# Kernel tuning notes

Measured on AMD Instinct MI355X. Metric: run time of the kernel, lower is better.

The kernel has to match this reference:

```python
import jax, jax.numpy as jnp
import numpy as np

B, S, D, H = 2, 4096, 128, 128
EPS = 1e-6
NEG_INF = -1e30


def _complex_linear(xr, xi, Wr, Wi, br, bi):
    # x: (B,S,D); W: (H,D); complex linear (Wr + i Wi)(xr + i xi) + (br + i bi) per layer math:
    # real_out = (xr Wr + br) - (xi Wi + bi); imag_out = (xi Wr + br) + (xr Wi + bi)
    out_r = xr @ Wr.T + br - (xi @ Wi.T + bi)
    out_i = xi @ Wr.T + br + (xr @ Wi.T + bi)
    return out_r, out_i


def setup_inputs() -> dict:
    key = jax.random.key(0)
    ks = jax.random.split(key, 24)
    scale = 1.0 / np.sqrt(D)
    def W(k):
        return jax.random.normal(k, (H, D), jnp.float32) * scale
    def b(k):
        return jax.random.normal(k, (H,), jnp.float32) * 0.01
    inp = {
        "Z_q": jax.random.normal(ks[0], (B, 2, S, D, 1), jnp.float32),
        "Z_k": jax.random.normal(ks[1], (B, 2, S, D, 1), jnp.float32),
        "Z_v": jax.random.normal(ks[2], (B, 2, S, D, 1), jnp.float32),
        "Wq_r": W(ks[3]), "Wq_i": W(ks[4]), "bq_r": b(ks[5]), "bq_i": b(ks[6]),
        "Wk_r": W(ks[7]), "Wk_i": W(ks[8]), "bk_r": b(ks[9]), "bk_i": b(ks[10]),
        "Wv_r": W(ks[11]), "Wv_i": W(ks[12]), "bv_r": b(ks[13]), "bv_i": b(ks[14]),
        "Wp_r": W(ks[15]), "Wp_i": W(ks[16]), "bp_r": b(ks[17]), "bp_i": b(ks[18]),
        "noise_floor": jnp.asarray(1.0, jnp.float32),
        "tau": jnp.asarray(0.0, jnp.float32),
    }
    return inp


def reference(Z_q, Z_k, Z_v,
              Wq_r, Wq_i, bq_r, bq_i,
              Wk_r, Wk_i, bk_r, bk_i,
              Wv_r, Wv_i, bv_r, bv_i,
              Wp_r, Wp_i, bp_r, bp_i,
              noise_floor, tau):
    # squeeze trailing singleton; split real/imag -> (B,S,D)
    zqr, zqi = Z_q[:, 0, :, :, 0], Z_q[:, 1, :, :, 0]
    zkr, zki = Z_k[:, 0, :, :, 0], Z_k[:, 1, :, :, 0]
    zvr, zvi = Z_v[:, 0, :, :, 0], Z_v[:, 1, :, :, 0]

    Qr, Qi = _complex_linear(zqr, zqi, Wq_r, Wq_i, bq_r, bq_i)
    Kr, Ki = _complex_linear(zkr, zki, Wk_r, Wk_i, bk_r, bk_i)
    Vr, Vi = _complex_linear(zvr, zvi, Wv_r, Wv_i, bv_r, bv_i)

    # InverseMahalanobis: R2[b,i,j] = sum_h |Q[b,i]-K[b,j]|^2
    q2 = jnp.sum(Qr * Qr + Qi * Qi, axis=-1)          # (B,S)
    k2 = jnp.sum(Kr * Kr + Ki * Ki, axis=-1)          # (B,S)
    re_qk = (jnp.einsum('bsh,bth->bst', Qr, Kr)
             + jnp.einsum('bsh,bth->bst', Qi, Ki))    # (B,S,S)
    R2 = q2[:, :, None] + k2[:, None, :] - 2.0 * re_qk

    attn_scores = -jax.nn.softplus(tau) * jnp.log(noise_floor ** 2 + R2 + EPS)
    mask = jnp.tril(jnp.ones((S, S), dtype=bool))[None]
    attn_scores = jnp.where(mask, attn_scores, NEG_INF)
    attn_weights = jax.nn.softmax(attn_scores / jnp.sqrt(jnp.float32(H)), axis=-1)

    # attn (real) times complex V
    est_r = jnp.einsum('bst,bth->bsh', attn_weights, Vr)
    est_i = jnp.einsum('bst,bth->bsh', attn_weights, Vi)

    out_r, out_i = _complex_linear(est_r, est_i, Wp_r, Wp_i, bp_r, bp_i)
    out = jnp.stack((out_r, out_i), axis=1)[..., None]  # (B,2,S,H,1)
    return out, attn_weights
```

## Files before the change

kernel.cpp:

```cpp
#include <hip/hip_runtime.h>

#define S_LEN 4096
#define NBATCH 2
#define ROWS (NBATCH*S_LEN)
#define OUT_ELEMS 2097152

typedef _Float16 f16;
typedef _Float16 f16x8 __attribute__((ext_vector_type(8)));
typedef _Float16 f16x4 __attribute__((ext_vector_type(4)));
typedef float f32x4 __attribute__((ext_vector_type(4)));

#define MT_OFF    0x000000
#define BIAS_OFF  0x080000
#define SC_OFF    0x081000
#define QH_OFF    0x100000
#define KH_OFF    0x500000
#define VT_OFF    0x900000
#define Q2_OFF    0xD00000
#define K2_OFF    0xD10000
#define L_OFF     0xD20000
#define EST_OFF   0xE00000
#define PW_OFF    0x1600000
#define WS_NEED   0x5600000

#define MFMA16(A,B,C) __builtin_amdgcn_mfma_f32_16x16x32_f16(A,B,C,0,0,0)

__device__ __forceinline__ void async_cp16(f16* lds, const f16* g) {
  __builtin_amdgcn_global_load_lds(
      (const __attribute__((address_space(1))) void*)g,
      (__attribute__((address_space(3))) void*)lds, 16, 0, 0);
}


template<int TR>
__device__ __forceinline__ void stage16(f16* lds, const f16* g, int stride, int tid) {
#pragma unroll
  for (int i = 0; i < TR/64; ++i) {
    int idx = i*256 + tid;
    int row = idx >> 2;
    int c = (idx & 3) ^ ((row >> 1) & 3);
    async_cp16(lds + idx*8, g + (size_t)row*stride + c*8);
  }
}

template<int TR>
__device__ __forceinline__ void stage32(f16* lds, const float* g, int stride, int tid,
                                        const float* rowscale) {
#pragma unroll
  for (int i = 0; i < TR/32; ++i) {
    int idx = i*256 + tid;
    int row = idx >> 3, c = idx & 7;
    const float4* gp = (const float4*)(g + (size_t)row*stride + c*4);
    float4 v = *gp;
    float sc = rowscale ? rowscale[row] : 1.0f;
    f16x4 h; h[0]=(f16)(v.x*sc); h[1]=(f16)(v.y*sc); h[2]=(f16)(v.z*sc); h[3]=(f16)(v.w*sc);
    int slot = (((c >> 1) ^ ((row >> 1) & 3)) << 3) + (c & 1)*4;
    *(f16x4*)(lds + row*32 + slot) = h;
  }
}

template<int MI, int NJ>
__device__ __forceinline__ void mfma_step(const f16* Asm, const f16* Bsm, int lane,
                                          int wm, int wn, f32x4 (&acc)[MI][NJ]) {
  f16x8 a[MI], b[NJ];
  int rr = lane & 15, kc = lane >> 4;
#pragma unroll
  for (int i=0;i<MI;i++) {
    int m = wm + i*16 + rr;
    a[i] = *(const f16x8*)(Asm + m*32 + ((kc ^ ((m>>1)&3)) << 3));
  }
#pragma unroll
  for (int j=0;j<NJ;j++) {
    int n = wn + j*16 + rr;
    b[j] = *(const f16x8*)(Bsm + n*32 + ((kc ^ ((n>>1)&3)) << 3));
  }
#pragma unroll
  for (int i=0;i<MI;i++)
#pragma unroll
    for (int j=0;j<NJ;j++) acc[i][j] = MFMA16(a[i], b[j], acc[i][j]);
}

__global__ __launch_bounds__(256)
void k_build(const float* Wqr, const float* Wqi, const float* bqr, const float* bqi,
             const float* Wkr, const float* Wki, const float* bkr, const float* bki,
             const float* Wvr, const float* Wvi, const float* bvr, const float* bvi,
             const float* Wpr, const float* Wpi, const float* bpr, const float* bpi,
             f16* Mt, float* bias) {
  int mat = blockIdx.x;
  const float *Wr, *Wi, *br, *bi;
  if (mat == 0)      { Wr=Wqr; Wi=Wqi; br=bqr; bi=bqi; }
  else if (mat == 1) { Wr=Wkr; Wi=Wki; br=bkr; bi=bki; }
  else if (mat == 2) { Wr=Wvr; Wi=Wvi; br=bvr; bi=bvi; }
  else               { Wr=Wpr; Wi=Wpi; br=bpr; bi=bpi; }
  int idx = blockIdx.y*256 + threadIdx.x;
  int n = idx >> 8, k = idx & 255;
  int d = k & 127, h = n & 127;
  float w = (k < 128) ? ((n < 128) ? Wr[h*128+d] : Wi[h*128+d])
                      : ((n < 128) ? -Wi[h*128+d] : Wr[h*128+d]);
  Mt[mat*65536 + n*256 + k] = (f16)w;
  if (k == 0)
    bias[mat*256 + n] = (n < 128) ? (br[n] - bi[n]) : (br[n-128] + bi[n-128]);
}

__global__ __launch_bounds__(256)
void k_init(float* est, float* zreg, float* sc, const float* nf, const float* tau) {
  int idx = blockIdx.x*256 + threadIdx.x;
  if (idx < 524288) ((float4*)est)[idx] = make_float4(0.f,0.f,0.f,0.f);
  else { int j = idx - 524288; if (j < 12288) ((float4*)zreg)[j] = make_float4(0.f,0.f,0.f,0.f); }
  if (idx == 0) {
    float t = tau[0];
    float c = __builtin_log2f(1.0f + __builtin_exp2f(t * 1.4426950408889634f))
              * 0.6931471805599453f;
    sc[0] = -c * 0.08838834764831845f;
    sc[1] = nf[0]*nf[0] + 1e-6f;
  }
}

__global__ __launch_bounds__(256)
void k_proj(const float* Zq, const float* Zk, const float* Zv,
            const f16* Mt, const float* bias,
            f16* Qh, f16* Kh, f16* Vt, float* q2, float* k2) {
  __shared__ f16 Asm[64*32];
  __shared__ f16 Bsm[128*32];
  __shared__ float bias_s[128];
  int tid = threadIdx.x;
  int mode = blockIdx.z;
  int m0 = blockIdx.x * 64, n0 = blockIdx.y * 128;
  const float* Z = (mode==0) ? Zq : (mode==1 ? Zk : Zv);
  const f16* Bt = Mt + mode*65536;
  if (tid < 128) bias_s[tid] = bias[mode*256 + n0 + tid];
  int b = m0 >> 12, s0 = m0 & 4095;
  int lane = tid & 63, w = tid >> 6;
  int wm = (w >> 1)*32, wn = (w & 1)*64;
  f32x4 acc[2][4] = {};
  for (int kb = 0; kb < 8; ++kb) {
    int k0 = kb*32;
    int part = k0 >> 7, d0 = k0 & 127;
    const float* Ag = Z + (((size_t)(b*2 + part))*S_LEN + s0)*128 + d0;
    stage32<64>(Asm, Ag, 128, tid, nullptr);
    stage16<128>(Bsm, Bt + n0*256 + k0, 256, tid);
    __syncthreads();
    mfma_step<2,4>(Asm, Bsm, lane, wm, wn, acc);
    __syncthreads();
  }
  int rr = (lane>>4)*4, cc = lane & 15;
  if (mode < 2) {
    f16* O = (mode==0) ? Qh : Kh;
    float rs[2][4];
#pragma unroll
    for (int i=0;i<2;i++)
#pragma unroll
      for (int r=0;r<4;r++) rs[i][r]=0.f;
#pragma unroll
    for (int i=0;i<2;i++)
#pragma unroll
      for (int j=0;j<4;j++) {
        int cl = wn + j*16 + cc;
        int cg = n0 + cl;
        float bv = bias_s[cl];
#pragma unroll
        for (int r=0;r<4;r++) {
          int rg = m0 + wm + i*16 + rr + r;
          f16 hv = (f16)(acc[i][j][r] + bv);
          O[(size_t)rg*256 + cg] = hv;
          float fv = (float)hv;
          rs[i][r] += fv*fv;
        }
      }
#pragma unroll
    for (int m=8;m>=1;m>>=1)
#pragma unroll
      for (int i=0;i<2;i++)
#pragma unroll
        for (int r=0;r<4;r++) rs[i][r] += __shfl_xor(rs[i][r], m, 64);
    if (cc == 0) {
      float* T = (mode==0) ? q2 : k2;
#pragma unroll
      for (int i=0;i<2;i++)
#pragma unroll
        for (int r=0;r<4;r++) {
          int rg = m0 + wm + i*16 + rr + r;
          atomicAdd(&T[rg], rs[i][r]);
        }
    }
  } else {
#pragma unroll
    for (int i=0;i<2;i++) {
      int t0 = s0 + wm + i*16 + rr;
#pragma unroll
      for (int j=0;j<4;j++) {
        int cl = wn + j*16 + cc;
        int cg = n0 + cl;
        float bv = bias_s[cl];
        f16x4 h4;
#pragma unroll
        for (int r=0;r<4;r++) h4[r] = (f16)(acc[i][j][r] + bv);
        *(f16x4*)(Vt + (size_t)b*1048576 + (size_t)cg*4096 + t0) = h4;
      }
    }
  }
}

__global__ __launch_bounds__(256)
void k_attn(const f16* Qh, const f16* Kh, const float* q2, const float* k2,
            const float* sc, float* lsum, f16* Pws) {
  __shared__ f16 Asm[128*32];
  __shared__ f16 Bsm[128*32];
  __shared__ float q2s[128], k2s[128];
  int x = blockIdx.x;
  int b = x / 528, r = x % 528;
  int sb = (int)((__builtin_sqrtf(8.f*(float)r + 1.f) - 1.f)*0.5f);
  while ((sb+1)*(sb+2)/2 <= r) sb++;
  while (sb*(sb+1)/2 > r) sb--;
  int tb = r - sb*(sb+1)/2;
  int s0 = sb*128, t0 = tb*128;
  int tid = threadIdx.x;
  if (tid < 128) {
    q2s[tid] = q2[b*S_LEN + s0 + tid];
    k2s[tid] = k2[b*S_LEN + t0 + tid];
  }
  float kc = sc[0], nf2 = sc[1];
  int lane = tid & 63, w = tid >> 6;
  int wm = (w >> 1)*64, wn = (w & 1)*64;
  const f16* Ag = Qh + ((size_t)(b*S_LEN) + s0)*256;
  const f16* Bg = Kh + ((size_t)(b*S_LEN) + t0)*256;
  f32x4 acc[4][4] = {};
  for (int kb=0;kb<8;kb++) {
    stage16<128>(Asm, Ag + kb*32, 256, tid);
    stage16<128>(Bsm, Bg + kb*32, 256, tid);
    __syncthreads();
    mfma_step<4,4>(Asm, Bsm, lane, wm, wn, acc);
    __syncthreads();
  }
  int rr = (lane>>4)*4, cc = lane & 15;
  bool diag = (tb == sb);
  float rs[4][4];
#pragma unroll
  for (int i=0;i<4;i++)
#pragma unroll
    for (int rg=0;rg<4;rg++) rs[i][rg]=0.f;
#pragma unroll
  for (int i=0;i<4;i++)
#pragma unroll
    for (int j=0;j<4;j++) {
      int cl = wn + j*16 + cc;
      float kv = k2s[cl];
#pragma unroll
      for (int rg=0;rg<4;rg++) {
        int rl = wm + i*16 + rr + rg;
        float xx = nf2 + q2s[rl] + kv - 2.0f*acc[i][j][rg];
        float P = __builtin_exp2f(kc * __builtin_log2f(__builtin_fmaxf(xx, 1e-6f)));
        if (diag && (t0+cl) > (s0+rl)) P = 0.f;
        Pws[((size_t)(b*S_LEN) + s0 + rl)*S_LEN + t0 + cl] = (f16)P;
        rs[i][rg] += P;
      }
    }
#pragma unroll
  for (int m=8;m>=1;m>>=1)
#pragma unroll
    for (int i=0;i<4;i++)
#pragma unroll
      for (int rg=0;rg<4;rg++) rs[i][rg] += __shfl_xor(rs[i][rg], m, 64);
  if (cc == 0)
#pragma unroll
    for (int i=0;i<4;i++)
#pragma unroll
      for (int rg=0;rg<4;rg++) {
        int rl = wm + i*16 + rr + rg;
        atomicAdd(&lsum[b*S_LEN + s0 + rl], rs[i][rg]);
      }
}

__global__ __launch_bounds__(256)
void k_pv(const f16* Pws, const f16* Vt, float* est) {
  __shared__ f16 Asm[128*32];
  __shared__ f16 Bsm[128*32];
  int r = blockIdx.x;
  int nb = blockIdx.y, b = blockIdx.z;
  int sb = 0;
  while (r >= ((sb+4)>>2)) { r -= (sb+4)>>2; sb++; }
  int c = r;
  int s0 = sb*128, h0 = nb*128;
  int tid = threadIdx.x;
  int lane = tid & 63, w = tid >> 6;
  int wm = (w>>1)*64, wn = (w&1)*64;
  int tb0 = c*4, tb1 = tb0 + 4; if (tb1 > sb+1) tb1 = sb+1;
  const f16* Abase = Pws + ((size_t)(b*S_LEN) + s0)*S_LEN;
  const f16* Bbase = Vt + (size_t)b*1048576 + (size_t)h0*4096;
  f32x4 acc[4][4] = {};
  for (int tb = tb0; tb < tb1; ++tb)
    for (int kk = 0; kk < 4; ++kk) {
      int t0 = tb*128 + kk*32;
      stage16<128>(Asm, Abase + t0, S_LEN, tid);
      stage16<128>(Bsm, Bbase + t0, 4096, tid);
      __syncthreads();
      mfma_step<4,4>(Asm, Bsm, lane, wm, wn, acc);
      __syncthreads();
    }
  int rr = (lane>>4)*4, cc = lane & 15;
#pragma unroll
  for (int i=0;i<4;i++)
#pragma unroll
    for (int j=0;j<4;j++) {
      int cg = h0 + wn + j*16 + cc;
#pragma unroll
      for (int rg=0;rg<4;rg++) {
        int rgl = s0 + wm + i*16 + rr + rg;
        atomicAdd(&est[((size_t)(b*S_LEN) + rgl)*256 + cg], acc[i][j][rg]);
      }
    }
}

__global__ __launch_bounds__(256)
void k_norm(const f16* __restrict__ Pws, const float* __restrict__ lsum,
            float* __restrict__ attn) {
  int base = blockIdx.x*1024 + threadIdx.x;
#pragma unroll
  for (int u = 0; u < 4; ++u) {
    int lin = base + u*256;
    int row = lin >> 10, t4 = lin & 1023;
    int srow = row & 4095;
    int t0 = t4 << 2;
    float4 o = make_float4(0.f,0.f,0.f,0.f);
    if (t0 <= srow) {
      float invl = 1.0f / lsum[row];
      f16x4 p = *(const f16x4*)(Pws + ((size_t)row<<12) + t0);
      o.x = (float)p[0]*invl;
      o.y = (t0+1 <= srow) ? (float)p[1]*invl : 0.f;
      o.z = (t0+2 <= srow) ? (float)p[2]*invl : 0.f;
      o.w = (t0+3 <= srow) ? (float)p[3]*invl : 0.f;
    }
    ((float4*)attn)[lin] = o;
  }
}

__global__ __launch_bounds__(256)
void k_out(const float* est, const f16* Mt, const float* bias, const float* lsum,
           float* outp) {
  __shared__ f16 Asm[64*32];
  __shared__ f16 Bsm[128*32];
  __shared__ float bias_s[128];
  __shared__ float ls[64];
  int m0 = blockIdx.x*64, n0 = blockIdx.y*128;
  int tid = threadIdx.x;
  int b = m0 >> 12, s0 = m0 & 4095;
  if (tid < 128) bias_s[tid] = bias[3*256 + n0 + tid];
  if (tid < 64)  ls[tid] = 1.0f / lsum[b*S_LEN + s0 + tid];
  __syncthreads();
  int lane = tid & 63, w = tid >> 6;
  int wm = (w>>1)*32, wn = (w&1)*64;
  const f16* Bt = Mt + 3*65536;
  f32x4 acc[2][4] = {};
  for (int kb=0;kb<8;kb++) {
    stage32<64>(Asm, est + (size_t)m0*256 + kb*32, 256, tid, ls);
    stage16<128>(Bsm, Bt + n0*256 + kb*32, 256, tid);
    __syncthreads();
    mfma_step<2,4>(Asm, Bsm, lane, wm, wn, acc);
    __syncthreads();
  }
  int rr = (lane>>4)*4, cc = lane & 15;
#pragma unroll
  for (int i=0;i<2;i++)
#pragma unroll
    for (int j=0;j<4;j++) {
      int cl = wn + j*16 + cc;
      int cg = n0 + cl;
      int comp = cg >> 7, h = cg & 127;
      float bv = bias_s[cl];
#pragma unroll
      for (int rg=0;rg<4;rg++) {
        int s = s0 + wm + i*16 + rr + rg;
        outp[(((size_t)(b*2 + comp))*S_LEN + s)*128 + h] = acc[i][j][rg] + bv;
      }
    }
}

extern "C" void kernel_launch(void* const* d_in, const int* in_sizes, int n_in,
                              void* d_out, int out_size, void* d_ws, size_t ws_size,
                              hipStream_t stream) {
  (void)in_sizes; (void)n_in; (void)out_size;
  if (ws_size < (size_t)WS_NEED) return;
  const float* Zq = (const float*)d_in[0];
  const float* Zk = (const float*)d_in[1];
  const float* Zv = (const float*)d_in[2];
  char* ws = (char*)d_ws;
  f16*   Mt   = (f16*)(ws + MT_OFF);
  float* bias = (float*)(ws + BIAS_OFF);
  float* sc   = (float*)(ws + SC_OFF);
  f16*   Qh   = (f16*)(ws + QH_OFF);
  f16*   Kh   = (f16*)(ws + KH_OFF);
  f16*   Vt   = (f16*)(ws + VT_OFF);
  float* q2   = (float*)(ws + Q2_OFF);
  float* k2   = (float*)(ws + K2_OFF);
  float* lsum = (float*)(ws + L_OFF);
  float* est  = (float*)(ws + EST_OFF);
  f16*   Pws  = (f16*)(ws + PW_OFF);
  float* outp = (float*)d_out;
  float* attn = outp + OUT_ELEMS;

  k_build<<<dim3(4,256), 256, 0, stream>>>(
      (const float*)d_in[3],  (const float*)d_in[4],  (const float*)d_in[5],  (const float*)d_in[6],
      (const float*)d_in[7],  (const float*)d_in[8],  (const float*)d_in[9],  (const float*)d_in[10],
      (const float*)d_in[11], (const float*)d_in[12], (const float*)d_in[13], (const float*)d_in[14],
      (const float*)d_in[15], (const float*)d_in[16], (const float*)d_in[17], (const float*)d_in[18],
      Mt, bias);
  k_init<<<2096, 256, 0, stream>>>(est, q2, sc, (const float*)d_in[19], (const float*)d_in[20]);
  k_proj<<<dim3(128,2,3), 256, 0, stream>>>(Zq, Zk, Zv, Mt, bias, Qh, Kh, Vt, q2, k2);
  k_attn<<<1056, 256, 0, stream>>>(Qh, Kh, q2, k2, sc, lsum, Pws);
  k_pv<<<dim3(144,2,2), 256, 0, stream>>>(Pws, Vt, est);
  k_norm<<<8192, 256, 0, stream>>>(Pws, lsum, attn);
  k_out<<<dim3(128,2), 256, 0, stream>>>(est, Mt, bias, lsum, outp);
}
```

Before: 308.3 us.

## Fuse attention normalization into PV kernel and replace atomics with split buffers

Row-sum atomics in the score kernel are replaced by per-tile partial sums reduced in a new small kernel. The PV kernel now uses chunks of 8 key blocks and writes non-atomically into up to four split est buffers, which the output projection sums while staging. The separate normalization pass is folded into the PV kernel, which writes normalized attention weights and the zero upper triangle. This removes atomics and one full pass over P, at the cost of a larger workspace, more zero-init traffic and more serialized work per block.

After: 334.4 us. 8.5% more time.

```diff
diff --git a/kernel.cpp b/kernel.cpp
--- a/kernel.cpp
+++ b/kernel.cpp
@@ -19,9 +19,10 @@
 #define Q2_OFF    0xD00000
 #define K2_OFF    0xD10000
 #define L_OFF     0xD20000
-#define EST_OFF   0xE00000
-#define PW_OFF    0x1600000
-#define WS_NEED   0x5600000
+#define RS_OFF    0xE00000
+#define EST_OFF   0x1200000
+#define PW_OFF    0x3200000
+#define WS_NEED   0x7200000
 
 #define MFMA16(A,B,C) __builtin_amdgcn_mfma_f32_16x16x32_f16(A,B,C,0,0,0)
 
@@ -30,7 +31,6 @@
       (const __attribute__((address_space(1))) void*)g,
       (__attribute__((address_space(3))) void*)lds, 16, 0, 0);
 }
-
 
 template<int TR>
 __device__ __forceinline__ void stage16(f16* lds, const f16* g, int stride, int tid) {
@@ -54,6 +54,28 @@
     float4 v = *gp;
     float sc = rowscale ? rowscale[row] : 1.0f;
     f16x4 h; h[0]=(f16)(v.x*sc); h[1]=(f16)(v.y*sc); h[2]=(f16)(v.z*sc); h[3]=(f16)(v.w*sc);
+    int slot = (((c >> 1) ^ ((row >> 1) & 3)) << 3) + (c & 1)*4;
+    *(f16x4*)(lds + row*32 + slot) = h;
+  }
+}
+
+__device__ __forceinline__ void stage32s4(f16* lds, const float* g, int tid,
+                                          const float* rowscale) {
+#pragma unroll
+  for (int i = 0; i < 2; ++i) {
+    int idx = i*256 + tid;
+    int row = idx >> 3, c = idx & 7;
+    const float4* p = (const float4*)(g + (size_t)row*256 + c*4);
+    float4 v0 = p[0];
+    float4 v1 = p[524288];
+    float4 v2 = p[1048576];
+    float4 v3 = p[1572864];
+    float sc = rowscale[row];
+    f16x4 h;
+    h[0]=(f16)((v0.x+v1.x+v2.x+v3.x)*sc);
+    h[1]=(f16)((v0.y+v1.y+v2.y+v3.y)*sc);
+    h[2]=(f16)((v0.z+v1.z+v2.z+v3.z)*sc);
+    h[3]=(f16)((v0.w+v1.w+v2.w+v3.w)*sc);
     int slot = (((c >> 1) ^ ((row >> 1) & 3)) << 3) + (c & 1)*4;
     *(f16x4*)(lds + row*32 + slot) = h;
   }
@@ -105,8 +127,8 @@
 __global__ __launch_bounds__(256)
 void k_init(float* est, float* zreg, float* sc, const float* nf, const float* tau) {
   int idx = blockIdx.x*256 + threadIdx.x;
-  if (idx < 524288) ((float4*)est)[idx] = make_float4(0.f,0.f,0.f,0.f);
-  else { int j = idx - 524288; if (j < 12288) ((float4*)zreg)[j] = make_float4(0.f,0.f,0.f,0.f); }
+  if (idx < 2097152) ((float4*)est)[idx] = make_float4(0.f,0.f,0.f,0.f);
+  else { int j = idx - 2097152; if (j < 12288) ((float4*)zreg)[j] = make_float4(0.f,0.f,0.f,0.f); }
   if (idx == 0) {
     float t = tau[0];
     float c = __builtin_log2f(1.0f + __builtin_exp2f(t * 1.4426950408889634f))
@@ -203,7 +225,7 @@
 
 __global__ __launch_bounds__(256)
 void k_attn(const f16* Qh, const f16* Kh, const float* q2, const float* k2,
-            const float* sc, float* lsum, f16* Pws) {
+            const float* sc, float* rsum, f16* Pws) {
   __shared__ f16 Asm[128*32];
   __shared__ f16 Bsm[128*32];
   __shared__ float q2s[128], k2s[128];
@@ -261,30 +283,41 @@
     for (int i=0;i<4;i++)
 #pragma unroll
       for (int rg=0;rg<4;rg++) rs[i][rg] += __shfl_xor(rs[i][rg], m, 64);
-  if (cc == 0)
+  if (cc == 0) {
+    float* R = rsum + ((size_t)((b*32+sb)*32+tb))*256 + (wn>>6)*128;
 #pragma unroll
     for (int i=0;i<4;i++)
 #pragma unroll
-      for (int rg=0;rg<4;rg++) {
-        int rl = wm + i*16 + rr + rg;
-        atomicAdd(&lsum[b*S_LEN + s0 + rl], rs[i][rg]);
-      }
-}
-
-__global__ __launch_bounds__(256)
-void k_pv(const f16* Pws, const f16* Vt, float* est) {
+      for (int rg=0;rg<4;rg++)
+        R[wm + i*16 + rr + rg] = rs[i][rg];
+  }
+}
+
+__global__ __launch_bounds__(256)
+void k_lred(const float* rsum, float* lsum) {
+  int s = blockIdx.x*256 + threadIdx.x;
+  int b = s >> 12, srow = s & 4095;
+  int sb = srow >> 7, rowin = srow & 127;
+  const float* R = rsum + ((size_t)((b*32+sb)*32))*256 + rowin;
+  float acc = 0.f;
+  for (int tb = 0; tb <= sb; ++tb) acc += R[tb*256] + R[tb*256+128];
+  lsum[s] = acc;
+}
+
+__global__ __launch_bounds__(256)
+void k_pv(const f16* Pws, const f16* Vt, const float* lsum, float* est, float* attn) {
   __shared__ f16 Asm[128*32];
   __shared__ f16 Bsm[128*32];
   int r = blockIdx.x;
   int nb = blockIdx.y, b = blockIdx.z;
   int sb = 0;
-  while (r >= ((sb+4)>>2)) { r -= (sb+4)>>2; sb++; }
+  while (r >= ((sb+8)>>3)) { r -= (sb+8)>>3; sb++; }
   int c = r;
   int s0 = sb*128, h0 = nb*128;
   int tid = threadIdx.x;
   int lane = tid & 63, w = tid >> 6;
   int wm = (w>>1)*64, wn = (w&1)*64;
-  int tb0 = c*4, tb1 = tb0 + 4; if (tb1 > sb+1) tb1 = sb+1;
+  int tb0 = c*8, tb1 = tb0 + 8; if (tb1 > sb+1) tb1 = sb+1;
   const f16* Abase = Pws + ((size_t)(b*S_LEN) + s0)*S_LEN;
   const f16* Bbase = Vt + (size_t)b*1048576 + (size_t)h0*4096;
   f32x4 acc[4][4] = {};
@@ -297,6 +330,7 @@
       mfma_step<4,4>(Asm, Bsm, lane, wm, wn, acc);
       __syncthreads();
     }
+  float* E = est + (size_t)c*2097152;
   int rr = (lane>>4)*4, cc = lane & 15;
 #pragma unroll
   for (int i=0;i<4;i++)
@@ -306,31 +340,32 @@
 #pragma unroll
       for (int rg=0;rg<4;rg++) {
         int rgl = s0 + wm + i*16 + rr + rg;
-        atomicAdd(&est[((size_t)(b*S_LEN) + rgl)*256 + cg], acc[i][j][rg]);
-      }
-    }
-}
-
-__global__ __launch_bounds__(256)
-void k_norm(const f16* __restrict__ Pws, const float* __restrict__ lsum,
-            float* __restrict__ attn) {
-  int base = blockIdx.x*1024 + threadIdx.x;
-#pragma unroll
-  for (int u = 0; u < 4; ++u) {
-    int lin = base + u*256;
-    int row = lin >> 10, t4 = lin & 1023;
-    int srow = row & 4095;
-    int t0 = t4 << 2;
-    float4 o = make_float4(0.f,0.f,0.f,0.f);
-    if (t0 <= srow) {
-      float invl = 1.0f / lsum[row];
-      f16x4 p = *(const f16x4*)(Pws + ((size_t)row<<12) + t0);
-      o.x = (float)p[0]*invl;
-      o.y = (t0+1 <= srow) ? (float)p[1]*invl : 0.f;
-      o.z = (t0+2 <= srow) ? (float)p[2]*invl : 0.f;
-      o.w = (t0+3 <= srow) ? (float)p[3]*invl : 0.f;
-    }
-    ((float4*)attn)[lin] = o;
+        E[((size_t)(b*S_LEN) + rgl)*256 + cg] = acc[i][j][rg];
+      }
+    }
+  if (nb == 0) {
+    int row = tid >> 1, half = tid & 1;
+    int s = s0 + row;
+    float invl = 1.0f / lsum[b*S_LEN + s];
+    for (int tb = tb0; tb < tb1; ++tb) {
+      int t0 = tb*128;
+      const f16* src = Pws + ((size_t)(b*S_LEN) + s)*S_LEN + t0 + half*64;
+      float4* dst = (float4*)(attn + ((size_t)(b*S_LEN) + s)*S_LEN + t0 + half*64);
+#pragma unroll
+      for (int u=0; u<8; ++u) {
+        f16x8 v = *(const f16x8*)(src + u*8);
+        float4 o0, o1;
+        o0.x=(float)v[0]*invl; o0.y=(float)v[1]*invl; o0.z=(float)v[2]*invl; o0.w=(float)v[3]*invl;
+        o1.x=(float)v[4]*invl; o1.y=(float)v[5]*invl; o1.z=(float)v[6]*invl; o1.w=(float)v[7]*invl;
+        dst[u*2] = o0; dst[u*2+1] = o1;
+      }
+      if (tb < sb) {
+        float4 z = make_float4(0.f,0.f,0.f,0.f);
+        float4* zd = (float4*)(attn + ((size_t)(b*S_LEN) + t0 + row)*S_LEN + s0 + half*64);
+#pragma unroll
+        for (int u=0; u<16; ++u) zd[u] = z;
+      }
+    }
   }
 }
 
@@ -352,7 +387,7 @@
   const f16* Bt = Mt + 3*65536;
   f32x4 acc[2][4] = {};
   for (int kb=0;kb<8;kb++) {
-    stage32<64>(Asm, est + (size_t)m0*256 + kb*32, 256, tid, ls);
+    stage32s4(Asm, est + (size_t)m0*256 + kb*32, tid, ls);
     stage16<128>(Bsm, Bt + n0*256 + kb*32, 256, tid);
     __syncthreads();
     mfma_step<2,4>(Asm, Bsm, lane, wm, wn, acc);
@@ -393,6 +428,7 @@
   float* q2   = (float*)(ws + Q2_OFF);
   float* k2   = (float*)(ws + K2_OFF);
   float* lsum = (float*)(ws + L_OFF);
+  float* rsum = (float*)(ws + RS_OFF);
   float* est  = (float*)(ws + EST_OFF);
   f16*   Pws  = (f16*)(ws + PW_OFF);
   float* outp = (float*)d_out;
@@ -404,10 +440,10 @@
       (const float*)d_in[11], (const float*)d_in[12], (const float*)d_in[13], (const float*)d_in[14],
       (const float*)d_in[15], (const float*)d_in[16], (const float*)d_in[17], (const float*)d_in[18],
       Mt, bias);
-  k_init<<<2096, 256, 0, stream>>>(est, q2, sc, (const float*)d_in[19], (const float*)d_in[20]);
+  k_init<<<8240, 256, 0, stream>>>(est, q2, sc, (const float*)d_in[19], (const float*)d_in[20]);
   k_proj<<<dim3(128,2,3), 256, 0, stream>>>(Zq, Zk, Zv, Mt, bias, Qh, Kh, Vt, q2, k2);
-  k_attn<<<1056, 256, 0, stream>>>(Qh, Kh, q2, k2, sc, lsum, Pws);
-  k_pv<<<dim3(144,2,2), 256, 0, stream>>>(Pws, Vt, est);
-  k_norm<<<8192, 256, 0, stream>>>(Pws, lsum, attn);
+  k_attn<<<1056, 256, 0, stream>>>(Qh, Kh, q2, k2, sc, rsum, Pws);
+  k_lred<<<32, 256, 0, stream>>>(rsum, lsum);
+  k_pv<<<dim3(80,2,2), 256, 0, stream>>>(Pws, Vt, lsum, est, attn);
   k_out<<<dim3(128,2), 256, 0, stream>>>(est, Mt, bias, lsum, outp);
 }
```

## Replace atomic reductions with partial buffers and separate reduction passes

Applied to the files above, without the earlier changes.

Row sums from the attention kernel are now written to per-tile partial slots and summed by a new small reduction kernel, replacing float atomics. The PV kernel splits the key range into chunks of two tiles (more blocks) and writes partial outputs to separate chunk buffers instead of atomically adding into a zeroed est, which also removes the large zero-init. The output projection now sums the chunk partials while staging its A tile, using 16-row blocks covering all 256 columns. This trades atomic traffic and init work for a much larger workspace and extra reads of partial buffers.

After: 355.4 us. 15.3% more time.

```diff
diff --git a/kernel.cpp b/kernel.cpp
--- a/kernel.cpp
+++ b/kernel.cpp
@@ -19,9 +19,10 @@
 #define Q2_OFF    0xD00000
 #define K2_OFF    0xD10000
 #define L_OFF     0xD20000
-#define EST_OFF   0xE00000
-#define PW_OFF    0x1600000
-#define WS_NEED   0x5600000
+#define RS_OFF    0xE00000
+#define EST_OFF   0x1200000
+#define PW_OFF    0x9200000
+#define WS_NEED   0xD200000
 
 #define MFMA16(A,B,C) __builtin_amdgcn_mfma_f32_16x16x32_f16(A,B,C,0,0,0)
 
@@ -30,7 +31,6 @@
       (const __attribute__((address_space(1))) void*)g,
       (__attribute__((address_space(3))) void*)lds, 16, 0, 0);
 }
-
 
 template<int TR>
 __device__ __forceinline__ void stage16(f16* lds, const f16* g, int stride, int tid) {
@@ -103,10 +103,9 @@
 }
 
 __global__ __launch_bounds__(256)
-void k_init(float* est, float* zreg, float* sc, const float* nf, const float* tau) {
+void k_init(float* zreg, float* sc, const float* nf, const float* tau) {
   int idx = blockIdx.x*256 + threadIdx.x;
-  if (idx < 524288) ((float4*)est)[idx] = make_float4(0.f,0.f,0.f,0.f);
-  else { int j = idx - 524288; if (j < 12288) ((float4*)zreg)[j] = make_float4(0.f,0.f,0.f,0.f); }
+  if (idx < 12288) ((float4*)zreg)[idx] = make_float4(0.f,0.f,0.f,0.f);
   if (idx == 0) {
     float t = tau[0];
     float c = __builtin_log2f(1.0f + __builtin_exp2f(t * 1.4426950408889634f))
@@ -203,7 +202,7 @@
 
 __global__ __launch_bounds__(256)
 void k_attn(const f16* Qh, const f16* Kh, const float* q2, const float* k2,
-            const float* sc, float* lsum, f16* Pws) {
+            const float* sc, float* rsum, f16* Pws) {
   __shared__ f16 Asm[128*32];
   __shared__ f16 Bsm[128*32];
   __shared__ float q2s[128], k2s[128];
@@ -261,14 +260,25 @@
     for (int i=0;i<4;i++)
 #pragma unroll
       for (int rg=0;rg<4;rg++) rs[i][rg] += __shfl_xor(rs[i][rg], m, 64);
-  if (cc == 0)
+  if (cc == 0) {
+    float* R = rsum + ((size_t)((b*32+sb)*32+tb))*256 + (wn>>6)*128;
 #pragma unroll
     for (int i=0;i<4;i++)
 #pragma unroll
-      for (int rg=0;rg<4;rg++) {
-        int rl = wm + i*16 + rr + rg;
-        atomicAdd(&lsum[b*S_LEN + s0 + rl], rs[i][rg]);
-      }
+      for (int rg=0;rg<4;rg++)
+        R[wm + i*16 + rr + rg] = rs[i][rg];
+  }
+}
+
+__global__ __launch_bounds__(256)
+void k_lred(const float* rsum, float* lsum) {
+  int s = blockIdx.x*256 + threadIdx.x;
+  int b = s >> 12, srow = s & 4095;
+  int sb = srow >> 7, rowin = srow & 127;
+  const float* R = rsum + ((size_t)((b*32+sb)*32))*256 + rowin;
+  float acc = 0.f;
+  for (int tb = 0; tb <= sb; ++tb) acc += R[tb*256] + R[tb*256+128];
+  lsum[s] = acc;
 }
 
 __global__ __launch_bounds__(256)
@@ -278,13 +288,13 @@
   int r = blockIdx.x;
   int nb = blockIdx.y, b = blockIdx.z;
   int sb = 0;
-  while (r >= ((sb+4)>>2)) { r -= (sb+4)>>2; sb++; }
+  while (r >= ((sb>>1)+1)) { r -= (sb>>1)+1; sb++; }
   int c = r;
   int s0 = sb*128, h0 = nb*128;
   int tid = threadIdx.x;
   int lane = tid & 63, w = tid >> 6;
   int wm = (w>>1)*64, wn = (w&1)*64;
-  int tb0 = c*4, tb1 = tb0 + 4; if (tb1 > sb+1) tb1 = sb+1;
+  int tb0 = c*2, tb1 = tb0 + 2; if (tb1 > sb+1) tb1 = sb+1;
   const f16* Abase = Pws + ((size_t)(b*S_LEN) + s0)*S_LEN;
   const f16* Bbase = Vt + (size_t)b*1048576 + (size_t)h0*4096;
   f32x4 acc[4][4] = {};
@@ -297,6 +307,7 @@
       mfma_step<4,4>(Asm, Bsm, lane, wm, wn, acc);
       __syncthreads();
     }
+  float* E = est + (size_t)c*2097152;
   int rr = (lane>>4)*4, cc = lane & 15;
 #pragma unroll
   for (int i=0;i<4;i++)
@@ -306,7 +317,7 @@
 #pragma unroll
       for (int rg=0;rg<4;rg++) {
         int rgl = s0 + wm + i*16 + rr + rg;
-        atomicAdd(&est[((size_t)(b*S_LEN) + rgl)*256 + cg], acc[i][j][rg]);
+        E[((size_t)(b*S_LEN) + rgl)*256 + cg] = acc[i][j][rg];
       }
     }
 }
@@ -337,42 +348,52 @@
 __global__ __launch_bounds__(256)
 void k_out(const float* est, const f16* Mt, const float* bias, const float* lsum,
            float* outp) {
-  __shared__ f16 Asm[64*32];
-  __shared__ f16 Bsm[128*32];
-  __shared__ float bias_s[128];
-  __shared__ float ls[64];
-  int m0 = blockIdx.x*64, n0 = blockIdx.y*128;
+  __shared__ f16 Asm[16*32];
+  __shared__ f16 Bsm[256*32];
+  __shared__ float bias_s[256];
+  __shared__ float ls[16];
+  int m0 = blockIdx.x*16;
   int tid = threadIdx.x;
   int b = m0 >> 12, s0 = m0 & 4095;
-  if (tid < 128) bias_s[tid] = bias[3*256 + n0 + tid];
-  if (tid < 64)  ls[tid] = 1.0f / lsum[b*S_LEN + s0 + tid];
+  int sb = s0 >> 7, nch = (sb>>1) + 1;
+  if (tid < 256) bias_s[tid] = bias[3*256 + tid];
+  if (tid < 16)  ls[tid] = 1.0f / lsum[b*S_LEN + s0 + tid];
   __syncthreads();
   int lane = tid & 63, w = tid >> 6;
-  int wm = (w>>1)*32, wn = (w&1)*64;
+  int wn = w*64;
   const f16* Bt = Mt + 3*65536;
-  f32x4 acc[2][4] = {};
+  f32x4 acc[1][4] = {};
   for (int kb=0;kb<8;kb++) {
-    stage32<64>(Asm, est + (size_t)m0*256 + kb*32, 256, tid, ls);
-    stage16<128>(Bsm, Bt + n0*256 + kb*32, 256, tid);
-    __syncthreads();
-    mfma_step<2,4>(Asm, Bsm, lane, wm, wn, acc);
+    if (tid < 128) {
+      int row = tid >> 3, c4 = tid & 7;
+      const float* basep = est + ((size_t)(b*S_LEN) + s0 + row)*256 + kb*32 + c4*4;
+      float4 v = make_float4(0.f,0.f,0.f,0.f);
+      for (int ch = 0; ch < nch; ++ch) {
+        float4 q = *(const float4*)(basep + (size_t)ch*2097152);
+        v.x += q.x; v.y += q.y; v.z += q.z; v.w += q.w;
+      }
+      float scl = ls[row];
+      f16x4 h; h[0]=(f16)(v.x*scl); h[1]=(f16)(v.y*scl); h[2]=(f16)(v.z*scl); h[3]=(f16)(v.w*scl);
+      int slot = (((c4 >> 1) ^ ((row >> 1) & 3)) << 3) + (c4 & 1)*4;
+      *(f16x4*)(Asm + row*32 + slot) = h;
+    }
+    stage16<256>(Bsm, Bt + kb*32, 256, tid);
+    __syncthreads();
+    mfma_step<1,4>(Asm, Bsm, lane, 0, wn, acc);
     __syncthreads();
   }
   int rr = (lane>>4)*4, cc = lane & 15;
 #pragma unroll
-  for (int i=0;i<2;i++)
-#pragma unroll
-    for (int j=0;j<4;j++) {
-      int cl = wn + j*16 + cc;
-      int cg = n0 + cl;
-      int comp = cg >> 7, h = cg & 127;
-      float bv = bias_s[cl];
-#pragma unroll
-      for (int rg=0;rg<4;rg++) {
-        int s = s0 + wm + i*16 + rr + rg;
-        outp[(((size_t)(b*2 + comp))*S_LEN + s)*128 + h] = acc[i][j][rg] + bv;
-      }
-    }
+  for (int j=0;j<4;j++) {
+    int cg = wn + j*16 + cc;
+    int comp = cg >> 7, h = cg & 127;
+    float bv = bias_s[cg];
+#pragma unroll
+    for (int rg=0;rg<4;rg++) {
+      int s = s0 + rr + rg;
+      outp[(((size_t)(b*2 + comp))*S_LEN + s)*128 + h] = acc[0][j][rg] + bv;
+    }
+  }
 }
 
 extern "C" void kernel_launch(void* const* d_in, const int* in_sizes, int n_in,
@@ -393,6 +414,7 @@
   float* q2   = (float*)(ws + Q2_OFF);
   float* k2   = (float*)(ws + K2_OFF);
   float* lsum = (float*)(ws + L_OFF);
+  float* rsum = (float*)(ws + RS_OFF);
   float* est  = (float*)(ws + EST_OFF);
   f16*   Pws  = (f16*)(ws + PW_OFF);
   float* outp = (float*)d_out;
@@ -404,10 +426,11 @@
       (const float*)d_in[11], (const float*)d_in[12], (const float*)d_in[13], (const float*)d_in[14],
       (const float*)d_in[15], (const float*)d_in[16], (const float*)d_in[17], (const float*)d_in[18],
       Mt, bias);
-  k_init<<<2096, 256, 0, stream>>>(est, q2, sc, (const float*)d_in[19], (const float*)d_in[20]);
+  k_init<<<48, 256, 0, stream>>>(q2, sc, (const float*)d_in[19], (const float*)d_in[20]);
   k_proj<<<dim3(128,2,3), 256, 0, stream>>>(Zq, Zk, Zv, Mt, bias, Qh, Kh, Vt, q2, k2);
-  k_attn<<<1056, 256, 0, stream>>>(Qh, Kh, q2, k2, sc, lsum, Pws);
-  k_pv<<<dim3(144,2,2), 256, 0, stream>>>(Pws, Vt, est);
+  k_attn<<<1056, 256, 0, stream>>>(Qh, Kh, q2, k2, sc, rsum, Pws);
+  k_lred<<<32, 256, 0, stream>>>(rsum, lsum);
+  k_pv<<<dim3(272,2,2), 256, 0, stream>>>(Pws, Vt, est);
   k_norm<<<8192, 256, 0, stream>>>(Pws, lsum, attn);
-  k_out<<<dim3(128,2), 256, 0, stream>>>(est, Mt, bias, lsum, outp);
-}
+  k_out<<<512, 256, 0, stream>>>(est, Mt, bias, lsum, outp);
+}
```
